# Performance work log

Hardware: AMD Instinct MI355X
Metric: run time of the kernel (lower is better)

## Reference

```python
import jax, jax.numpy as jnp
import numpy as np

D_MODEL = 1024
D_K = 64
D_V = 64
H = 16
B = 4
S = 2048
NEG = -1000000000.0


def setup_inputs() -> dict:
    key = jax.random.key(0)
    ks = jax.random.split(key, 6)
    x = jax.random.normal(ks[0], (B, S, D_MODEL), dtype=jnp.float32)
    # mask: 1 = pad, 0 = valid (per module's `mask = 1 - mask` convention)
    mask = jax.random.randint(ks[1], (B, S), 0, 2, dtype=jnp.int32)
    sc = 1.0 / np.sqrt(D_MODEL)
    Wq = jax.random.normal(ks[2], (D_K * H, D_MODEL), dtype=jnp.float32) * sc
    Wk = jax.random.normal(ks[3], (D_K * H, D_MODEL), dtype=jnp.float32) * sc
    Wv = jax.random.normal(ks[4], (D_V * H, D_MODEL), dtype=jnp.float32) * sc
    Wo = jax.random.normal(ks[5], (D_MODEL, D_V * H), dtype=jnp.float32) * (1.0 / np.sqrt(D_V * H))
    return {"x": x, "mask": mask, "Wq": Wq, "Wk": Wk, "Wv": Wv, "Wo": Wo}


def _split_heads(y, h):
    b, s, _ = y.shape
    return y.reshape(b, s, h, -1).transpose(0, 2, 1, 3)  # [B,H,S,d]


def reference(x, mask, Wq, Wk, Wv, Wo):
    # valid = 1 - mask (1 where token is valid); bidirectional pad mask = outer product
    valid = (1 - mask).astype(x.dtype)  # [B,S]
    pair = valid[:, None, :, None] * valid[:, None, None, :]  # [B,1,S,S]
    q = _split_heads(x @ Wq.T, H)  # [B,H,S,dk]
    k = _split_heads(x @ Wk.T, H)
    v = _split_heads(x @ Wv.T, H)
    qk = jnp.einsum("bhqd,bhkd->bhqk", q, k) / jnp.sqrt(jnp.asarray(D_K, x.dtype))
    qk = jnp.where(pair == 0, jnp.asarray(NEG, x.dtype), qk)
    attn = jax.nn.softmax(qk, axis=-1)  # dropout omitted (eval mode)
    heads = jnp.einsum("bhqk,bhkd->bhqd", attn, v)
    concat = heads.transpose(0, 2, 1, 3).reshape(x.shape[0], x.shape[1], -1)
    return concat @ Wo.T
```

## Files before the change

### kernel.cpp

```cpp
#include <hip/hip_runtime.h>
#include <stdint.h>


typedef __bf16 bf16;
typedef __bf16 bf16x8 __attribute__((ext_vector_type(8)));
typedef __bf16 bf16x4 __attribute__((ext_vector_type(4)));
typedef float f32x4 __attribute__((ext_vector_type(4)));
typedef float f32x16 __attribute__((ext_vector_type(16)));

#define DM    1024
#define NH    16
#define SS    2048
#define BB    4
#define NTOK  8192
#define QKVLD 3072
#define LOG2E_DIV8 0.18033688011112042f

__device__ __forceinline__ int swz(int row, int byteoff) {
    return byteoff ^ ((row & 7) << 4);
}
__device__ __forceinline__ float fexp2(float x) {
    float r; asm("v_exp_f32 %0, %1" : "=v"(r) : "v"(x)); return r;
}
__device__ __forceinline__ uint32_t cvtpk(float lo, float hi_) {
    uint32_t r; asm("v_cvt_pk_bf16_f32 %0, %1, %2" : "=v"(r) : "v"(lo), "v"(hi_)); return r;
}
__device__ __forceinline__ void gload_lds16(const void* g, void* l) {
    __builtin_amdgcn_global_load_lds(
        (const __attribute__((address_space(1))) uint32_t*)g,
        (__attribute__((address_space(3))) uint32_t*)l, 16, 0, 0);
}

__global__ void cvt_kernel(const float* __restrict__ in, bf16* __restrict__ out, int n8) {
    int i = blockIdx.x * blockDim.x + threadIdx.x;
    if (i >= n8) return;
    const float4* p = reinterpret_cast<const float4*>(in) + (size_t)i * 2;
    float4 a = p[0], b = p[1];
    bf16x8 o;
    o[0] = (bf16)a.x; o[1] = (bf16)a.y; o[2] = (bf16)a.z; o[3] = (bf16)a.w;
    o[4] = (bf16)b.x; o[5] = (bf16)b.y; o[6] = (bf16)b.z; o[7] = (bf16)b.w;
    reinterpret_cast<bf16x8*>(out)[i] = o;
}

__global__ void wcvt_kernel(const float* __restrict__ wq, const float* __restrict__ wk,
                            const float* __restrict__ wv, const float* __restrict__ wo,
                            bf16* __restrict__ wqkv, bf16* __restrict__ wob) {
    int i = blockIdx.x * blockDim.x + threadIdx.x;
    int seg = i >> 17, off = i & 131071;
    const float* src = (seg == 0) ? wq : (seg == 1) ? wk : (seg == 2) ? wv : wo;
    bf16* dst = (seg < 3) ? (wqkv + (size_t)seg * DM * DM) : wob;
    const float4* p = reinterpret_cast<const float4*>(src) + (size_t)off * 2;
    float4 a = p[0], b = p[1];
    bf16x8 o;
    o[0] = (bf16)a.x; o[1] = (bf16)a.y; o[2] = (bf16)a.z; o[3] = (bf16)a.w;
    o[4] = (bf16)b.x; o[5] = (bf16)b.y; o[6] = (bf16)b.z; o[7] = (bf16)b.w;
    reinterpret_cast<bf16x8*>(dst)[off] = o;
}

__global__ void biasprep_kernel(const int* __restrict__ mask, float* __restrict__ bias) {
    int idx = blockIdx.x * blockDim.x + threadIdx.x;
    if (idx >= 5 * 2048) return;
    int e = idx & 15, hi = (idx >> 4) & 1, hs = (idx >> 5) & 1;
    int kt = (idx >> 6) & 31, b = idx >> 11;
    int key = 32 * hs + 4 * hi + 8 * (e >> 2) + (e & 3);
    float v = 0.f;
    if (b < 4 && mask[b * SS + kt * 64 + key]) v = -__builtin_inff();
    bias[idx] = v;
}

template <typename OT>
__global__ __launch_bounds__(256) void gemm_bt(
    const bf16* __restrict__ A, int lda, const bf16* __restrict__ Bm, OT* __restrict__ C,
    int M, int N, int K)
{
    __shared__ bf16 As[128 * 64];
    __shared__ bf16 Bs[128 * 64];

    const int nwg = gridDim.x * gridDim.y;
    const int wg = blockIdx.y * gridDim.x + blockIdx.x;
    const int nsw = (wg & 7) * (nwg >> 3) + (wg >> 3);
    const int tn = nsw % gridDim.x, tm = nsw / gridDim.x;

    const int tid = threadIdx.x;
    const int lane = tid & 63, wv = tid >> 6;
    const int wr = wv >> 1, wc = wv & 1;
    const int lr = lane & 15, lg = lane >> 4;

    const f32x4 zero = {0.f, 0.f, 0.f, 0.f};
    f32x4 acc[4][4];
#pragma unroll
    for (int mi = 0; mi < 4; ++mi)
#pragma unroll
        for (int ni = 0; ni < 4; ++ni) acc[mi][ni] = zero;

    const char* Abase = (const char*)(A + (size_t)(tm * 128) * lda);
    const char* Bbase = (const char*)(Bm + (size_t)(tn * 128) * K);

    for (int k0 = 0; k0 < K; k0 += 64) {
#pragma unroll
        for (int i = 0; i < 4; ++i) {
            int idx = tid + 256 * i;
            int row = idx >> 3, ch = idx & 7;
            int gcol = (ch * 16) ^ ((row & 7) << 4);
            gload_lds16(Abase + (size_t)row * (lda * 2) + k0 * 2 + gcol, (char*)As + idx * 16);
            gload_lds16(Bbase + (size_t)row * (K * 2) + k0 * 2 + gcol, (char*)Bs + idx * 16);
        }
        __syncthreads();

#pragma unroll
        for (int ks = 0; ks < 2; ++ks) {
            bf16x8 af[4], bfr[4];
#pragma unroll
            for (int mi = 0; mi < 4; ++mi) {
                int row = wr * 64 + mi * 16 + lr;
                af[mi] = *reinterpret_cast<const bf16x8*>(
                    (char*)As + swz(row, row * 128 + ks * 64 + lg * 16));
            }
#pragma unroll
            for (int ni = 0; ni < 4; ++ni) {
                int row = wc * 64 + ni * 16 + lr;
                bfr[ni] = *reinterpret_cast<const bf16x8*>(
                    (char*)Bs + swz(row, row * 128 + ks * 64 + lg * 16));
            }
#pragma unroll
            for (int mi = 0; mi < 4; ++mi)
#pragma unroll
                for (int ni = 0; ni < 4; ++ni)
                    acc[mi][ni] = __builtin_amdgcn_mfma_f32_16x16x32_bf16(
                        af[mi], bfr[ni], acc[mi][ni], 0, 0, 0);
        }
        __syncthreads();
    }

#pragma unroll
    for (int mi = 0; mi < 4; ++mi)
#pragma unroll
        for (int ni = 0; ni < 4; ++ni)
#pragma unroll
            for (int r = 0; r < 4; ++r) {
                int row = tm * 128 + wr * 64 + mi * 16 + lg * 4 + r;
                int col = tn * 128 + wc * 64 + ni * 16 + lr;
                C[(size_t)row * N + col] = (OT)acc[mi][ni][r];
            }
}

__global__ __launch_bounds__(256) void vtrans_kernel(
    const bf16* __restrict__ vb, int ldv, bf16* __restrict__ vT)
{
    const int st = blockIdx.x, bh = blockIdx.y;
    const int b = bh >> 4, h = bh & 15;
    const int tid = threadIdx.x;
    __shared__ bf16 T[64 * 64];
#pragma unroll
    for (int i = 0; i < 2; ++i) {
        int idx = tid + 256 * i;
        int s = idx >> 3, ch = idx & 7;
        bf16x8 v = *reinterpret_cast<const bf16x8*>(
            vb + (size_t)(b * SS + st * 64 + s) * ldv + h * 64 + ch * 8);
        *reinterpret_cast<bf16x8*>((char*)T + swz(s, s * 128 + ch * 16)) = v;
    }
    __syncthreads();
#pragma unroll
    for (int i = 0; i < 2; ++i) {
        int idx = tid + 256 * i;
        int d = idx >> 3, ch = idx & 7;
        bf16x8 o;
#pragma unroll
        for (int j = 0; j < 8; ++j) {
            int s = ch * 8 + j;
            o[j] = *reinterpret_cast<const bf16*>((char*)T + swz(s, s * 128 + d * 2));
        }
        *reinterpret_cast<bf16x8*>(vT + ((size_t)bh * 64 + d) * SS + st * 64 + ch * 8) = o;
    }
}

__global__ __launch_bounds__(256) void attn_kernel(
    const bf16* __restrict__ qkv, const bf16* __restrict__ vT,
    const float* __restrict__ bias, const int* __restrict__ mask,
    bf16* __restrict__ concat)
{
    const int w = blockIdx.x;
    const int nw = (w & 7) * 128 + (w >> 3);
    const int qt = nw & 15, bh = nw >> 4;
    const int b = bh >> 4, h = bh & 15;
    const int tid = threadIdx.x;
    const int lane = tid & 63, wv = tid >> 6;
    const int lq = lane & 31, hi = lane >> 5;

    __shared__ bf16 Ks[2][64 * 64];
    __shared__ bf16 Vs[2][64 * 64];

    const size_t tok0 = (size_t)b * SS;
    const int qrow0 = qt * 128 + wv * 32;

    const int qpad = mask[tok0 + qrow0 + lq];
    bf16x8 qf[4];
    {
        const bf16* qp = qkv + (tok0 + qrow0 + lq) * QKVLD + h * 64 + hi * 8;
#pragma unroll
        for (int ks = 0; ks < 4; ++ks) {
            bf16x8 v = *reinterpret_cast<const bf16x8*>(qp + ks * 16);
#pragma unroll
            for (int j = 0; j < 8; ++j)
                v[j] = qpad ? (bf16)0.f : (bf16)((float)v[j] * LOG2E_DIV8);
            qf[ks] = v;
        }
    }
    const float* bbase = bias + (size_t)(qpad ? 4 : b) * 2048 + hi * 16;

    float mrow = -3e38f, lrow = 0.f;
    f32x16 oA, oB;
#pragma unroll
    for (int e = 0; e < 16; ++e) { oA[e] = 0.f; oB[e] = 0.f; }

    const int srow[2] = { tid >> 3, (tid + 256) >> 3 };
    const int sch[2]  = { tid & 7, tid & 7 };
    const bf16* kbase = qkv + 1024 + h * 64;
    const int cx = (hi * 16) ^ ((lq & 7) << 4);

    bf16x8 stK[2], stV[2];
#pragma unroll
    for (int i = 0; i < 2; ++i) {
        stK[i] = *reinterpret_cast<const bf16x8*>(
            kbase + (tok0 + srow[i]) * QKVLD + sch[i] * 8);
        stV[i] = *reinterpret_cast<const bf16x8*>(
            vT + ((size_t)bh * 64 + srow[i]) * SS + sch[i] * 8);
    }
#pragma unroll
    for (int i = 0; i < 2; ++i) {
        *reinterpret_cast<bf16x8*>((char*)Ks[0] + swz(srow[i], srow[i] * 128 + sch[i] * 16)) = stK[i];
        *reinterpret_cast<bf16x8*>((char*)Vs[0] + swz(srow[i], srow[i] * 128 + sch[i] * 16)) = stV[i];
    }
    __syncthreads();

    for (int kt = 0; kt < 32; ++kt) {
        const int cur = kt & 1;
        if (kt < 31) {
#pragma unroll
            for (int i = 0; i < 2; ++i) {
                stK[i] = *reinterpret_cast<const bf16x8*>(
                    kbase + (tok0 + (kt + 1) * 64 + srow[i]) * QKVLD + sch[i] * 8);
                stV[i] = *reinterpret_cast<const bf16x8*>(
                    vT + ((size_t)bh * 64 + srow[i]) * SS + (kt + 1) * 64 + sch[i] * 8);
            }
        }
        const char* kB = (const char*)Ks[cur];
        const char* vB = (const char*)Vs[cur];
        const int off0 = lq * 128 + cx, off1 = (32 + lq) * 128 + cx;

        f32x16 s0 = *reinterpret_cast<const f32x16*>(bbase + kt * 64);
        f32x16 s1 = *reinterpret_cast<const f32x16*>(bbase + kt * 64 + 32);
        __builtin_amdgcn_s_setprio(1);
#pragma unroll
        for (int ks = 0; ks < 4; ++ks) {
            bf16x8 k0 = *reinterpret_cast<const bf16x8*>(kB + (off0 ^ (ks * 32)));
            bf16x8 k1 = *reinterpret_cast<const bf16x8*>(kB + (off1 ^ (ks * 32)));
            s0 = __builtin_amdgcn_mfma_f32_32x32x16_bf16(k0, qf[ks], s0, 0, 0, 0);
            s1 = __builtin_amdgcn_mfma_f32_32x32x16_bf16(k1, qf[ks], s1, 0, 0, 0);
        }
        __builtin_amdgcn_s_setprio(0);

        float pm = fmaxf(s0[0], s0[1]);
#pragma unroll
        for (int e = 2; e < 16; e += 2) pm = fmaxf(pm, fmaxf(s0[e], s0[e + 1]));
#pragma unroll
        for (int e = 0; e < 16; e += 2) pm = fmaxf(pm, fmaxf(s1[e], s1[e + 1]));
        pm = fmaxf(pm, __shfl_xor(pm, 32));

        if (!__all(pm <= mrow + 11.0f)) {
            float mnew = fmaxf(mrow, pm);
            float scf = fexp2(mrow - mnew);
            mrow = mnew;
            lrow *= scf;
#pragma unroll
            for (int e = 0; e < 16; ++e) { oA[e] *= scf; oB[e] *= scf; }
        }

        float p0[16], p1[16];
        float ps0 = 0.f, ps1 = 0.f, ps2 = 0.f, ps3 = 0.f;
#pragma unroll
        for (int e = 0; e < 16; e += 2) {
            p0[e] = fexp2(s0[e] - mrow);     ps0 += p0[e];
            p0[e + 1] = fexp2(s0[e + 1] - mrow); ps1 += p0[e + 1];
            p1[e] = fexp2(s1[e] - mrow);     ps2 += p1[e];
            p1[e + 1] = fexp2(s1[e + 1] - mrow); ps3 += p1[e + 1];
        }
        float psum = (ps0 + ps1) + (ps2 + ps3);
        psum += __shfl_xor(psum, 32);
        lrow += psum;

        __builtin_amdgcn_s_setprio(1);
#pragma unroll
        for (int kk = 0; kk < 4; ++kk) {
            const float* pp = (kk < 2) ? p0 : p1;
            const int ks2 = kk & 1;
            uint32_t c0 = cvtpk(pp[8 * ks2 + 0], pp[8 * ks2 + 1]);
            uint32_t c1 = cvtpk(pp[8 * ks2 + 2], pp[8 * ks2 + 3]);
            uint32_t c2 = cvtpk(pp[8 * ks2 + 4], pp[8 * ks2 + 5]);
            uint32_t c3 = cvtpk(pp[8 * ks2 + 6], pp[8 * ks2 + 7]);
            asm("v_permlane32_swap_b32 %0, %1" : "+v"(c0), "+v"(c2));
            asm("v_permlane32_swap_b32 %0, %1" : "+v"(c1), "+v"(c3));
            union { uint32_t u[4]; bf16x8 v; } pu;
            pu.u[0] = c0; pu.u[1] = c1; pu.u[2] = c2; pu.u[3] = c3;
            bf16x8 vf0 = *reinterpret_cast<const bf16x8*>(vB + (off0 ^ (kk * 32)));
            bf16x8 vf1 = *reinterpret_cast<const bf16x8*>(vB + (off1 ^ (kk * 32)));
            oA = __builtin_amdgcn_mfma_f32_32x32x16_bf16(vf0, pu.v, oA, 0, 0, 0);
            oB = __builtin_amdgcn_mfma_f32_32x32x16_bf16(vf1, pu.v, oB, 0, 0, 0);
        }
        __builtin_amdgcn_s_setprio(0);

        if (kt < 31) {
#pragma unroll
            for (int i = 0; i < 2; ++i) {
                *reinterpret_cast<bf16x8*>(
                    (char*)Ks[cur ^ 1] + swz(srow[i], srow[i] * 128 + sch[i] * 16)) = stK[i];
                *reinterpret_cast<bf16x8*>(
                    (char*)Vs[cur ^ 1] + swz(srow[i], srow[i] * 128 + sch[i] * 16)) = stV[i];
            }
            __syncthreads();
        }
    }

    float inv = 1.0f / lrow;
#pragma unroll
    for (int g = 0; g < 4; ++g) {
        bf16x4 w0, w1;
#pragma unroll
        for (int r = 0; r < 4; ++r) {
            w0[r] = (bf16)(oA[g * 4 + r] * inv);
            w1[r] = (bf16)(oB[g * 4 + r] * inv);
        }
        int d0 = 4 * hi + 8 * g;
        bf16* cp = concat + (tok0 + qrow0 + lq) * QKVLD + h * 64 + d0;
        *reinterpret_cast<bf16x4*>(cp) = w0;
        *reinterpret_cast<bf16x4*>(cp + 32) = w1;
    }
}

extern "C" void kernel_launch(void* const* d_in, const int* in_sizes, int n_in,
                              void* d_out, int out_size, void* d_ws, size_t ws_size,
                              hipStream_t stream)
{
    const float* x  = (const float*)d_in[0];
    const int* mask = (const int*)d_in[1];
    const float* Wq = (const float*)d_in[2];
    const float* Wk = (const float*)d_in[3];
    const float* Wv = (const float*)d_in[4];
    const float* Wo = (const float*)d_in[5];
    float* out = (float*)d_out;

    char* ws = (char*)d_ws;
    bf16* xb    = (bf16*)(ws);
    bf16* wqkv  = (bf16*)(ws + (16ull << 20));
    bf16* wob   = (bf16*)(ws + (22ull << 20));
    bf16* qkv   = (bf16*)(ws + (24ull << 20));
    bf16* vT    = xb;
    float* bias = (float*)wqkv;
    bf16* concat = qkv + 2048;

    cvt_kernel<<<dim3((NTOK * DM / 8) / 256), 256, 0, stream>>>(x, xb, NTOK * DM / 8);
    wcvt_kernel<<<dim3(2048), 256, 0, stream>>>(Wq, Wk, Wv, Wo, wqkv, wob);

    gemm_bt<bf16><<<dim3(QKVLD / 128, NTOK / 128), 256, 0, stream>>>(
        xb, DM, wqkv, qkv, NTOK, QKVLD, DM);

    vtrans_kernel<<<dim3(SS / 64, BB * NH), 256, 0, stream>>>(qkv + 2048, QKVLD, vT);
    biasprep_kernel<<<dim3(40), 256, 0, stream>>>(mask, bias);

    attn_kernel<<<dim3((SS / 128) * (BB * NH)), 256, 0, stream>>>(
        qkv, vT, bias, mask, concat);

    gemm_bt<float><<<dim3(DM / 128, NTOK / 128), 256, 0, stream>>>(
        concat, QKVLD, wob, out, NTOK, DM, DM);
}
```

Baseline: 234.5 us.

## Stream K/V tiles straight into LDS with direct global-to-LDS loads

The attention kernel's double-buffered K and V tile prefetch now uses direct global-to-LDS 16-byte loads instead of staging through registers and then writing to LDS. The XOR swizzle moves from the LDS destination address to the global source address, so each lane writes a contiguous LDS slot and the layout stays the same. The bias load is hoisted ahead of the prefetch. This is meant to free the staging registers and drop the explicit LDS store pass, but it relies on the barrier waiting for the outstanding vector-memory loads before the buffer is read.

New measurement: 226.6 us. -3.4%, faster.

```diff
diff --git a/kernel.cpp b/kernel.cpp
--- a/kernel.cpp
+++ b/kernel.cpp
@@ -213,43 +213,44 @@
 #pragma unroll
     for (int e = 0; e < 16; ++e) { oA[e] = 0.f; oB[e] = 0.f; }
 
-    const int srow[2] = { tid >> 3, (tid + 256) >> 3 };
-    const int sch[2]  = { tid & 7, tid & 7 };
-    const bf16* kbase = qkv + 1024 + h * 64;
+    const int srow = tid >> 3, sch = tid & 7;
+    const int srow2 = (tid + 256) >> 3;
+    const int gc1 = (sch * 16) ^ ((srow & 7) << 4);
+    const int gc2 = (sch * 16) ^ ((srow2 & 7) << 4);
+    const char* kSrc = (const char*)(qkv + 1024 + h * 64);
+    const char* vSrc = (const char*)(vT + (size_t)bh * 64 * SS);
+    const size_t kOff1 = (tok0 + srow) * (QKVLD * 2) + gc1;
+    const size_t kOff2 = (tok0 + srow2) * (QKVLD * 2) + gc2;
+    const size_t vOff1 = (size_t)srow * (SS * 2) + gc1;
+    const size_t vOff2 = (size_t)srow2 * (SS * 2) + gc2;
+    const int ldsOff1 = tid * 16, ldsOff2 = (tid + 256) * 16;
     const int cx = (hi * 16) ^ ((lq & 7) << 4);
 
-    bf16x8 stK[2], stV[2];
-#pragma unroll
-    for (int i = 0; i < 2; ++i) {
-        stK[i] = *reinterpret_cast<const bf16x8*>(
-            kbase + (tok0 + srow[i]) * QKVLD + sch[i] * 8);
-        stV[i] = *reinterpret_cast<const bf16x8*>(
-            vT + ((size_t)bh * 64 + srow[i]) * SS + sch[i] * 8);
-    }
-#pragma unroll
-    for (int i = 0; i < 2; ++i) {
-        *reinterpret_cast<bf16x8*>((char*)Ks[0] + swz(srow[i], srow[i] * 128 + sch[i] * 16)) = stK[i];
-        *reinterpret_cast<bf16x8*>((char*)Vs[0] + swz(srow[i], srow[i] * 128 + sch[i] * 16)) = stV[i];
-    }
+    gload_lds16(kSrc + kOff1, (char*)Ks[0] + ldsOff1);
+    gload_lds16(kSrc + kOff2, (char*)Ks[0] + ldsOff2);
+    gload_lds16(vSrc + vOff1, (char*)Vs[0] + ldsOff1);
+    gload_lds16(vSrc + vOff2, (char*)Vs[0] + ldsOff2);
     __syncthreads();
 
     for (int kt = 0; kt < 32; ++kt) {
         const int cur = kt & 1;
+
+        f32x16 s0 = *reinterpret_cast<const f32x16*>(bbase + kt * 64);
+        f32x16 s1 = *reinterpret_cast<const f32x16*>(bbase + kt * 64 + 32);
+
         if (kt < 31) {
-#pragma unroll
-            for (int i = 0; i < 2; ++i) {
-                stK[i] = *reinterpret_cast<const bf16x8*>(
-                    kbase + (tok0 + (kt + 1) * 64 + srow[i]) * QKVLD + sch[i] * 8);
-                stV[i] = *reinterpret_cast<const bf16x8*>(
-                    vT + ((size_t)bh * 64 + srow[i]) * SS + (kt + 1) * 64 + sch[i] * 8);
-            }
-        }
+            const size_t kAdv = (size_t)(kt + 1) * 64 * (QKVLD * 2);
+            const size_t vAdv = (size_t)(kt + 1) * 128;
+            gload_lds16(kSrc + kOff1 + kAdv, (char*)Ks[cur ^ 1] + ldsOff1);
+            gload_lds16(kSrc + kOff2 + kAdv, (char*)Ks[cur ^ 1] + ldsOff2);
+            gload_lds16(vSrc + vOff1 + vAdv, (char*)Vs[cur ^ 1] + ldsOff1);
+            gload_lds16(vSrc + vOff2 + vAdv, (char*)Vs[cur ^ 1] + ldsOff2);
+        }
+
         const char* kB = (const char*)Ks[cur];
         const char* vB = (const char*)Vs[cur];
         const int off0 = lq * 128 + cx, off1 = (32 + lq) * 128 + cx;
 
-        f32x16 s0 = *reinterpret_cast<const f32x16*>(bbase + kt * 64);
-        f32x16 s1 = *reinterpret_cast<const f32x16*>(bbase + kt * 64 + 32);
         __builtin_amdgcn_s_setprio(1);
 #pragma unroll
         for (int ks = 0; ks < 4; ++ks) {
@@ -309,16 +310,7 @@
         }
         __builtin_amdgcn_s_setprio(0);
 
-        if (kt < 31) {
-#pragma unroll
-            for (int i = 0; i < 2; ++i) {
-                *reinterpret_cast<bf16x8*>(
-                    (char*)Ks[cur ^ 1] + swz(srow[i], srow[i] * 128 + sch[i] * 16)) = stK[i];
-                *reinterpret_cast<bf16x8*>(
-                    (char*)Vs[cur ^ 1] + swz(srow[i], srow[i] * 128 + sch[i] * 16)) = stV[i];
-            }
-            __syncthreads();
-        }
+        if (kt < 31) __syncthreads();
     }
 
     float inv = 1.0f / lrow;
```
